# Performance work log

Measured on AMD Instinct MI355X. Metric: run time of the kernel, lower is better.

The kernel has to match this reference:

```python
import math
import jax, jax.numpy as jnp
import numpy as np

N = 100000      # nodes
E = 3200000     # edges (avg degree 32)
NFEAT = 512
NH = 256
NC = 40
NL = 8
ALPHA = 0.1
LAMDA = 0.5


def setup_inputs() -> dict:
    key = jax.random.key(0)
    ks = jax.random.split(key, 9)
    features = jax.random.normal(ks[0], (N, NFEAT), jnp.float32)
    edge_rows = jax.random.randint(ks[1], (E,), 0, N, jnp.int32)
    edge_cols = jax.random.randint(ks[2], (E,), 0, N, jnp.int32)
    # scale by 1/avg_degree so aggregated features stay O(1) (mimics normalized adjacency)
    edge_vals = jax.random.uniform(ks[3], (E,), jnp.float32) / 32.0
    # fcs[0]: nn.Linear(nfeat, nhidden) default init U(-1/sqrt(in), 1/sqrt(in))
    b1 = 1.0 / math.sqrt(NFEAT)
    W_in = jax.random.uniform(ks[4], (NFEAT, NH), jnp.float32, -b1, b1)
    b_in = jax.random.uniform(ks[5], (NH,), jnp.float32, -b1, b1)
    # GraphConvolution weights: U(-1/sqrt(out), 1/sqrt(out))
    bw = 1.0 / math.sqrt(NH)
    conv_weights = jax.random.uniform(ks[6], (NL, NH, NH), jnp.float32, -bw, bw)
    # fcs[1]: nn.Linear(nhidden, nclass)
    b2 = 1.0 / math.sqrt(NH)
    W_out = jax.random.uniform(ks[7], (NH, NC), jnp.float32, -b2, b2)
    b_out = jax.random.uniform(ks[8], (NC,), jnp.float32, -b2, b2)
    return {
        "features": features,
        "edge_rows": edge_rows,
        "edge_cols": edge_cols,
        "edge_vals": edge_vals,
        "W_in": W_in,
        "b_in": b_in,
        "conv_weights": conv_weights,
        "W_out": W_out,
        "b_out": b_out,
    }


def reference(features, edge_rows, edge_cols, edge_vals, W_in, b_in, conv_weights, W_out, b_out):
    # dropout p=0 in eval -> identity
    h = jax.nn.relu(features @ W_in + b_in)  # [N, NH]
    h0 = h
    for i in range(NL):
        theta = math.log(LAMDA / (i + 1) + 1.0)
        # SpMM: hi = G @ h via gather + segment-sum over destination rows
        hi = jax.ops.segment_sum(edge_vals[:, None] * h[edge_cols], edge_rows, num_segments=N)
        support = (1.0 - ALPHA) * hi + ALPHA * h0  # variant=False -> r == support
        h = jax.nn.relu(theta * (support @ conv_weights[i]) + (1.0 - theta) * support)
    return h @ W_out + b_out  # [N, NC]
```

## Files before the change

kernel.cpp:

```cpp
#include <hip/hip_runtime.h>
#include <hip/hip_fp16.h>
#include <math.h>

#define NNODE   100000
#define NEDGE   3200000
#define NFEAT   512
#define NH      256
#define NC      40
#define NL      8

#define SCAN_B  256

typedef _Float16 f16x8 __attribute__((ext_vector_type(8)));
typedef float    f32x4 __attribute__((ext_vector_type(4)));

__global__ void count_deg_kernel(const int* __restrict__ rows, int* __restrict__ deg, int e) {
    int i = blockIdx.x * blockDim.x + threadIdx.x;
    if (i < e) atomicAdd(&deg[rows[i]], 1);
}

__global__ void scan_pass1(const int* __restrict__ deg, int* __restrict__ rowptr,
                           int* __restrict__ bsums, int n) {
    __shared__ int sm[SCAN_B];
    int i = blockIdx.x * SCAN_B + threadIdx.x;
    int v = (i < n) ? deg[i] : 0;
    sm[threadIdx.x] = v;
    __syncthreads();
    for (int off = 1; off < SCAN_B; off <<= 1) {
        int t = (threadIdx.x >= (unsigned)off) ? sm[threadIdx.x - off] : 0;
        __syncthreads();
        sm[threadIdx.x] += t;
        __syncthreads();
    }
    if (i < n) rowptr[i] = sm[threadIdx.x] - v;
    if (threadIdx.x == SCAN_B - 1) bsums[blockIdx.x] = sm[threadIdx.x];
}

__global__ void scan_pass2(int* __restrict__ bsums, int nb) {
    __shared__ int sm[512];
    int tid = threadIdx.x;
    int v = (tid < nb) ? bsums[tid] : 0;
    sm[tid] = v;
    __syncthreads();
    for (int off = 1; off < 512; off <<= 1) {
        int t = (tid >= off) ? sm[tid - off] : 0;
        __syncthreads();
        sm[tid] += t;
        __syncthreads();
    }
    if (tid < nb) bsums[tid] = sm[tid] - v;
}

__global__ void scan_pass3(int* __restrict__ rowptr, const int* __restrict__ bsums,
                           int* __restrict__ cursor, int n, int total) {
    int i = blockIdx.x * blockDim.x + threadIdx.x;
    if (i < n) {
        int v = rowptr[i] + bsums[i / SCAN_B];
        rowptr[i] = v;
        cursor[i] = v;
    }
    if (i == 0) rowptr[n] = total;
}

__global__ void scatter_edges_kernel(const int* __restrict__ rows, const int* __restrict__ cols,
                                     const float* __restrict__ vals, int* __restrict__ cursor,
                                     int* __restrict__ csr_col, float* __restrict__ csr_val, int e) {
    int i = blockIdx.x * blockDim.x + threadIdx.x;
    if (i < e) {
        int r = rows[i];
        int p = atomicAdd(&cursor[r], 1);
        csr_col[p] = cols[i];
        csr_val[p] = vals[i];
    }
}

__device__ inline float4 dec8(uint2 p) {
    __half2 h01 = *(__half2*)&p.x;
    __half2 h23 = *(__half2*)&p.y;
    float2 f01 = __half22float2(h01);
    float2 f23 = __half22float2(h23);
    return make_float4(f01.x, f01.y, f23.x, f23.y);
}

__device__ inline void gload16(const void* g, void* l) {
    __builtin_amdgcn_global_load_lds((const __attribute__((address_space(1))) void*)g,
                                     (__attribute__((address_space(3))) void*)l,
                                     16, 0, 0);
}

__global__ void convert_f2h4(const float* __restrict__ in, __half* __restrict__ out, long n4) {
    long stride = (long)gridDim.x * blockDim.x;
    for (long i = (long)blockIdx.x * blockDim.x + threadIdx.x; i < n4; i += stride) {
        float4 f = ((const float4*)in)[i];
        __half2 a = __floats2half2_rn(f.x, f.y);
        __half2 b = __floats2half2_rn(f.z, f.w);
        uint2 pk;
        pk.x = *(unsigned*)&a;
        pk.y = *(unsigned*)&b;
        ((uint2*)out)[i] = pk;
    }
}

__global__ void convert_win(const float* __restrict__ in, __half* __restrict__ out) {
    int idx = blockIdx.x * blockDim.x + threadIdx.x;
    if (idx < NFEAT * NH) {
        int k = idx >> 8;
        int n = idx & 255;
        out[n * NFEAT + k] = __float2half(in[idx]);
    }
}

__global__ void convert_convw(const float* __restrict__ in, __half* __restrict__ out) {
    int idx = blockIdx.x * blockDim.x + threadIdx.x;
    if (idx < NL * NH * NH) {
        int l = idx >> 16;
        int rem = idx & 65535;
        int k = rem >> 8;
        int n = rem & 255;
        out[(size_t)l * 65536 + n * 256 + k] = __float2half(in[idx]);
    }
}

__global__ __launch_bounds__(256) void spmm_kernel(
    const int* __restrict__ rowptr, const int* __restrict__ csr_col,
    const float* __restrict__ csr_val, const __half* __restrict__ h16,
    const __half* __restrict__ h016,
    float* __restrict__ sup32, __half* __restrict__ sup16, int n)
{
    int lane = threadIdx.x & 63;
    int r = blockIdx.x * 4 + (threadIdx.x >> 6);
    if (r >= n) return;
    int e0 = rowptr[r], e1 = rowptr[r + 1];
    const uint2* hv = (const uint2*)h16;
    float4 acc = make_float4(0.f, 0.f, 0.f, 0.f);
    int e = e0;
    for (; e + 4 <= e1; e += 4) {
        int   c0 = csr_col[e],     c1 = csr_col[e + 1];
        int   c2 = csr_col[e + 2], c3 = csr_col[e + 3];
        float v0 = csr_val[e],     v1 = csr_val[e + 1];
        float v2 = csr_val[e + 2], v3 = csr_val[e + 3];
        uint2 p0 = hv[(size_t)c0 * 64 + lane];
        uint2 p1 = hv[(size_t)c1 * 64 + lane];
        uint2 p2 = hv[(size_t)c2 * 64 + lane];
        uint2 p3 = hv[(size_t)c3 * 64 + lane];
        float4 x0 = dec8(p0), x1 = dec8(p1), x2 = dec8(p2), x3 = dec8(p3);
        acc.x += v0 * x0.x + v1 * x1.x + v2 * x2.x + v3 * x3.x;
        acc.y += v0 * x0.y + v1 * x1.y + v2 * x2.y + v3 * x3.y;
        acc.z += v0 * x0.z + v1 * x1.z + v2 * x2.z + v3 * x3.z;
        acc.w += v0 * x0.w + v1 * x1.w + v2 * x2.w + v3 * x3.w;
    }
    for (; e < e1; ++e) {
        int c = csr_col[e];
        float v = csr_val[e];
        float4 x = dec8(hv[(size_t)c * 64 + lane]);
        acc.x += v * x.x; acc.y += v * x.y; acc.z += v * x.z; acc.w += v * x.w;
    }
    float4 s0 = dec8(((const uint2*)h016)[(size_t)r * 64 + lane]);
    float4 o;
    o.x = 0.9f * acc.x + 0.1f * s0.x;
    o.y = 0.9f * acc.y + 0.1f * s0.y;
    o.z = 0.9f * acc.z + 0.1f * s0.z;
    o.w = 0.9f * acc.w + 0.1f * s0.w;
    ((float4*)sup32)[(size_t)r * 64 + lane] = o;
    __half2 ha = __floats2half2_rn(o.x, o.y);
    __half2 hb = __floats2half2_rn(o.z, o.w);
    uint2 pk;
    pk.x = *(unsigned*)&ha;
    pk.y = *(unsigned*)&hb;
    ((uint2*)sup16)[(size_t)r * 64 + lane] = pk;
}

__global__ __launch_bounds__(256) void mfma_gemm(
    const __half* __restrict__ A, const __half* __restrict__ BT,
    const float* __restrict__ bias, const float* __restrict__ Csrc32,
    __half* __restrict__ out16, int M, int K,
    float theta, float omt, int mode)
{
    __shared__ __align__(16) char smem[32768];
    const int tid  = threadIdx.x;
    const int lane = tid & 63;
    const int w    = tid >> 6;
    const int wr   = w >> 1, wc = w & 1;
    const int bm0  = blockIdx.x * 128;
    const int bn0  = blockIdx.y * 128;
    const size_t strideAB = (size_t)K * 2;

    f32x4 acc[4][4];
    #pragma unroll
    for (int m = 0; m < 4; ++m)
        #pragma unroll
        for (int n = 0; n < 4; ++n)
            acc[m][n] = (f32x4)0.f;

    auto stage = [&](int kt, int buf) {
        const long k0b = (long)kt * 64;
        #pragma unroll
        for (int i = 0; i < 2; ++i) {
            int ia  = w * 2 + i;
            int row = ia * 16 + (lane >> 2);
            int q   = (lane & 3) * 16;
            int qs  = q ^ (((row >> 1) & 3) << 4);
            {
                int grow = bm0 + row; if (grow >= M) grow = M - 1;
                const char* g = (const char*)A + (size_t)grow * strideAB + k0b + qs;
                char* l = smem + buf * 16384 + ia * 1024;
                gload16(g, l);
            }
            {
                int gcol = bn0 + row;
                const char* g = (const char*)BT + (size_t)gcol * strideAB + k0b + qs;
                char* l = smem + buf * 16384 + 8192 + ia * 1024;
                gload16(g, l);
            }
        }
    };

    auto compute = [&](int buf) {
        const char* As = smem + buf * 16384;
        const char* Bs = As + 8192;
        const int q = (lane >> 4) * 16;
        f16x8 af[4], bf[4];
        #pragma unroll
        for (int m = 0; m < 4; ++m) {
            int row = wr * 64 + m * 16 + (lane & 15);
            af[m] = *(const f16x8*)(As + row * 64 + (q ^ (((row >> 1) & 3) << 4)));
        }
        #pragma unroll
        for (int n = 0; n < 4; ++n) {
            int col = wc * 64 + n * 16 + (lane & 15);
            bf[n] = *(const f16x8*)(Bs + col * 64 + (q ^ (((col >> 1) & 3) << 4)));
        }
        #pragma unroll
        for (int m = 0; m < 4; ++m)
            #pragma unroll
            for (int n = 0; n < 4; ++n)
                acc[m][n] = __builtin_amdgcn_mfma_f32_16x16x32_f16(af[m], bf[n], acc[m][n], 0, 0, 0);
    };

    const int nkt = K >> 5;
    stage(0, 0);
    __syncthreads();
    for (int kt = 0; kt < nkt; ++kt) {
        if (kt + 1 < nkt) stage(kt + 1, (kt + 1) & 1);
        compute(kt & 1);
        __syncthreads();
    }

    #pragma unroll
    for (int m = 0; m < 4; ++m) {
        int rbase = bm0 + wr * 64 + m * 16 + (lane >> 4) * 4;
        #pragma unroll
        for (int r = 0; r < 4; ++r) {
            int grow = rbase + r;
            if (grow >= M) continue;
            #pragma unroll
            for (int n = 0; n < 4; ++n) {
                int gcol = bn0 + wc * 64 + n * 16 + (lane & 15);
                float x = acc[m][n][r];
                if (mode == 0) {
                    x = fmaxf(x + bias[gcol], 0.f);
                } else {
                    x = fmaxf(theta * x + omt * Csrc32[(size_t)grow * 256 + gcol], 0.f);
                }
                out16[(size_t)grow * 256 + gcol] = __float2half(x);
            }
        }
    }
}

#define BM 128
#define BN 64
#define BK 16

__global__ __launch_bounds__(256) void gemm_out_kernel(
    const __half* __restrict__ A16, const float* __restrict__ B,
    const float* __restrict__ bias, float* __restrict__ out32,
    int M, int Nn, int K)
{
    __shared__ float As[BK][BM + 4];
    __shared__ float Bs[BK][BN + 4];
    int tid = threadIdx.x;
    int tx = tid & 15;
    int ty = tid >> 4;
    int bm0 = blockIdx.x * BM;
    int bn0 = blockIdx.y * BN;

    float acc[8][4];
    #pragma unroll
    for (int i = 0; i < 8; ++i)
        #pragma unroll
        for (int j = 0; j < 4; ++j) acc[i][j] = 0.f;

    for (int k0 = 0; k0 < K; k0 += BK) {
        #pragma unroll
        for (int r = 0; r < 2; ++r) {
            int idx = tid + r * 256;
            int m   = idx >> 2;
            int kk  = (idx & 3) * 4;
            int gm  = bm0 + m;
            float4 f = make_float4(0.f, 0.f, 0.f, 0.f);
            if (gm < M) f = dec8(*(const uint2*)&A16[(size_t)gm * K + k0 + kk]);
            As[kk + 0][m] = f.x;
            As[kk + 1][m] = f.y;
            As[kk + 2][m] = f.z;
            As[kk + 3][m] = f.w;
        }
        {
            int kk = tid >> 4;
            int n4 = (tid & 15) * 4;
            int gn = bn0 + n4;
            const float* brow = &B[(size_t)(k0 + kk) * Nn];
            float t0 = (gn + 0 < Nn) ? brow[gn + 0] : 0.f;
            float t1 = (gn + 1 < Nn) ? brow[gn + 1] : 0.f;
            float t2 = (gn + 2 < Nn) ? brow[gn + 2] : 0.f;
            float t3 = (gn + 3 < Nn) ? brow[gn + 3] : 0.f;
            Bs[kk][n4 + 0] = t0;
            Bs[kk][n4 + 1] = t1;
            Bs[kk][n4 + 2] = t2;
            Bs[kk][n4 + 3] = t3;
        }
        __syncthreads();
        #pragma unroll
        for (int kk = 0; kk < BK; ++kk) {
            float a[8], b[4];
            #pragma unroll
            for (int i = 0; i < 8; ++i) a[i] = As[kk][ty * 8 + i];
            #pragma unroll
            for (int j = 0; j < 4; ++j) b[j] = Bs[kk][tx * 4 + j];
            #pragma unroll
            for (int i = 0; i < 8; ++i)
                #pragma unroll
                for (int j = 0; j < 4; ++j)
                    acc[i][j] += a[i] * b[j];
        }
        __syncthreads();
    }

    #pragma unroll
    for (int i = 0; i < 8; ++i) {
        int m = bm0 + ty * 8 + i;
        if (m >= M) continue;
        int n0 = bn0 + tx * 4;
        #pragma unroll
        for (int j = 0; j < 4; ++j) {
            int n = n0 + j;
            if (n < Nn) out32[(size_t)m * Nn + n] = acc[i][j] + bias[n];
        }
    }
}

extern "C" void kernel_launch(void* const* d_in, const int* in_sizes, int n_in,
                              void* d_out, int out_size, void* d_ws, size_t ws_size,
                              hipStream_t stream) {
    const float* features = (const float*)d_in[0];
    const int*   erows    = (const int*)d_in[1];
    const int*   ecols    = (const int*)d_in[2];
    const float* evals    = (const float*)d_in[3];
    const float* W_in     = (const float*)d_in[4];
    const float* b_in     = (const float*)d_in[5];
    const float* convW    = (const float*)d_in[6];
    const float* W_out    = (const float*)d_in[7];
    const float* b_out    = (const float*)d_in[8];
    float* out = (float*)d_out;

    const int n = NNODE;
    const int e = NEDGE;

    char* w = (char*)d_ws;
    auto alloc = [&](size_t bytes) -> void* {
        void* p = (void*)w;
        w += (bytes + 255) & ~(size_t)255;
        return p;
    };
    float*  sup32   = (float*)alloc((size_t)n * NH * 4);
    __half* feat16  = (__half*)sup32;
    __half* h0_16   = (__half*)alloc((size_t)n * NH * 2);
    __half* hb_16   = (__half*)alloc((size_t)n * NH * 2);
    __half* sup16   = (__half*)alloc((size_t)n * NH * 2);
    __half* WtIn16  = (__half*)alloc((size_t)NFEAT * NH * 2);
    __half* convWt16= (__half*)alloc((size_t)NL * NH * NH * 2);
    int*    rowptr  = (int*)alloc((size_t)(n + 1) * 4);
    int*    cursor  = (int*)alloc((size_t)n * 4);
    int*    bsums   = (int*)alloc(4096 * 4);
    int*    csr_col = (int*)alloc((size_t)e * 4);
    float*  csr_val = (float*)alloc((size_t)e * 4);

    hipMemsetAsync(cursor, 0, (size_t)n * 4, stream);
    count_deg_kernel<<<(e + 255) / 256, 256, 0, stream>>>(erows, cursor, e);
    int nb = (n + SCAN_B - 1) / SCAN_B;
    scan_pass1<<<nb, SCAN_B, 0, stream>>>(cursor, rowptr, bsums, n);
    scan_pass2<<<1, 512, 0, stream>>>(bsums, nb);
    scan_pass3<<<nb, SCAN_B, 0, stream>>>(rowptr, bsums, cursor, n, e);
    scatter_edges_kernel<<<(e + 255) / 256, 256, 0, stream>>>(
        erows, ecols, evals, cursor, csr_col, csr_val, e);

    convert_f2h4<<<2048, 256, 0, stream>>>(features, feat16, (long)n * NFEAT / 4);
    convert_win<<<(NFEAT * NH + 255) / 256, 256, 0, stream>>>(W_in, WtIn16);
    convert_convw<<<(NL * NH * NH + 255) / 256, 256, 0, stream>>>(convW, convWt16);

    dim3 gmm((n + 127) / 128, 2);
    mfma_gemm<<<gmm, 256, 0, stream>>>(feat16, WtIn16, b_in, nullptr,
                                       h0_16, n, NFEAT, 0.f, 0.f, 0);

    const __half* hcur16 = h0_16;
    for (int i = 0; i < NL; ++i) {
        spmm_kernel<<<(n + 3) / 4, 256, 0, stream>>>(rowptr, csr_col, csr_val,
                                                     hcur16, h0_16, sup32, sup16, n);
        double th = log(0.5 / (double)(i + 1) + 1.0);
        mfma_gemm<<<gmm, 256, 0, stream>>>(sup16, convWt16 + (size_t)i * NH * NH,
                                           nullptr, sup32, hb_16,
                                           n, NH, (float)th, (float)(1.0 - th), 1);
        hcur16 = hb_16;
    }

    dim3 gout((n + BM - 1) / BM, (NC + BN - 1) / BN);
    gemm_out_kernel<<<gout, 256, 0, stream>>>(hb_16, W_out, b_out, out, n, NC, NH);
}
```

Before: 3.500 ms.

## Fuse feature conversion into GEMM, interleave CSR col/val, drop fp32 support buffer

The input GEMM now reads fp32 features directly and converts them to fp16 while staging into LDS. This removes the separate conversion kernel and its 100MB round trip. CSR column and value arrays are interleaved into int2 so each edge needs one load. The SpMM no longer writes an fp32 copy of support, and the GEMM epilogue reads the fp16 copy instead, which cuts about 100MB of traffic per layer at the cost of some precision in the residual term.

```diff
diff --git a/kernel.cpp b/kernel.cpp
--- a/kernel.cpp
+++ b/kernel.cpp
@@ -64,13 +64,12 @@
 
 __global__ void scatter_edges_kernel(const int* __restrict__ rows, const int* __restrict__ cols,
                                      const float* __restrict__ vals, int* __restrict__ cursor,
-                                     int* __restrict__ csr_col, float* __restrict__ csr_val, int e) {
+                                     int2* __restrict__ csr_cv, int e) {
     int i = blockIdx.x * blockDim.x + threadIdx.x;
     if (i < e) {
         int r = rows[i];
         int p = atomicAdd(&cursor[r], 1);
-        csr_col[p] = cols[i];
-        csr_val[p] = vals[i];
+        csr_cv[p] = make_int2(cols[i], __float_as_int(vals[i]));
     }
 }
 
@@ -86,19 +85,6 @@
     __builtin_amdgcn_global_load_lds((const __attribute__((address_space(1))) void*)g,
                                      (__attribute__((address_space(3))) void*)l,
                                      16, 0, 0);
-}
-
-__global__ void convert_f2h4(const float* __restrict__ in, __half* __restrict__ out, long n4) {
-    long stride = (long)gridDim.x * blockDim.x;
-    for (long i = (long)blockIdx.x * blockDim.x + threadIdx.x; i < n4; i += stride) {
-        float4 f = ((const float4*)in)[i];
-        __half2 a = __floats2half2_rn(f.x, f.y);
-        __half2 b = __floats2half2_rn(f.z, f.w);
-        uint2 pk;
-        pk.x = *(unsigned*)&a;
-        pk.y = *(unsigned*)&b;
-        ((uint2*)out)[i] = pk;
-    }
 }
 
 __global__ void convert_win(const float* __restrict__ in, __half* __restrict__ out) {
@@ -122,10 +108,9 @@
 }
 
 __global__ __launch_bounds__(256) void spmm_kernel(
-    const int* __restrict__ rowptr, const int* __restrict__ csr_col,
-    const float* __restrict__ csr_val, const __half* __restrict__ h16,
-    const __half* __restrict__ h016,
-    float* __restrict__ sup32, __half* __restrict__ sup16, int n)
+    const int* __restrict__ rowptr, const int2* __restrict__ csr_cv,
+    const __half* __restrict__ h16, const __half* __restrict__ h016,
+    __half* __restrict__ sup16, int n)
 {
     int lane = threadIdx.x & 63;
     int r = blockIdx.x * 4 + (threadIdx.x >> 6);
@@ -135,14 +120,14 @@
     float4 acc = make_float4(0.f, 0.f, 0.f, 0.f);
     int e = e0;
     for (; e + 4 <= e1; e += 4) {
-        int   c0 = csr_col[e],     c1 = csr_col[e + 1];
-        int   c2 = csr_col[e + 2], c3 = csr_col[e + 3];
-        float v0 = csr_val[e],     v1 = csr_val[e + 1];
-        float v2 = csr_val[e + 2], v3 = csr_val[e + 3];
-        uint2 p0 = hv[(size_t)c0 * 64 + lane];
-        uint2 p1 = hv[(size_t)c1 * 64 + lane];
-        uint2 p2 = hv[(size_t)c2 * 64 + lane];
-        uint2 p3 = hv[(size_t)c3 * 64 + lane];
+        int2 a0 = csr_cv[e],     a1 = csr_cv[e + 1];
+        int2 a2 = csr_cv[e + 2], a3 = csr_cv[e + 3];
+        float v0 = __int_as_float(a0.y), v1 = __int_as_float(a1.y);
+        float v2 = __int_as_float(a2.y), v3 = __int_as_float(a3.y);
+        uint2 p0 = hv[(size_t)a0.x * 64 + lane];
+        uint2 p1 = hv[(size_t)a1.x * 64 + lane];
+        uint2 p2 = hv[(size_t)a2.x * 64 + lane];
+        uint2 p3 = hv[(size_t)a3.x * 64 + lane];
         float4 x0 = dec8(p0), x1 = dec8(p1), x2 = dec8(p2), x3 = dec8(p3);
         acc.x += v0 * x0.x + v1 * x1.x + v2 * x2.x + v3 * x3.x;
         acc.y += v0 * x0.y + v1 * x1.y + v2 * x2.y + v3 * x3.y;
@@ -150,9 +135,9 @@
         acc.w += v0 * x0.w + v1 * x1.w + v2 * x2.w + v3 * x3.w;
     }
     for (; e < e1; ++e) {
-        int c = csr_col[e];
-        float v = csr_val[e];
-        float4 x = dec8(hv[(size_t)c * 64 + lane]);
+        int2 a = csr_cv[e];
+        float v = __int_as_float(a.y);
+        float4 x = dec8(hv[(size_t)a.x * 64 + lane]);
         acc.x += v * x.x; acc.y += v * x.y; acc.z += v * x.z; acc.w += v * x.w;
     }
     float4 s0 = dec8(((const uint2*)h016)[(size_t)r * 64 + lane]);
@@ -161,7 +146,6 @@
     o.y = 0.9f * acc.y + 0.1f * s0.y;
     o.z = 0.9f * acc.z + 0.1f * s0.z;
     o.w = 0.9f * acc.w + 0.1f * s0.w;
-    ((float4*)sup32)[(size_t)r * 64 + lane] = o;
     __half2 ha = __floats2half2_rn(o.x, o.y);
     __half2 hb = __floats2half2_rn(o.z, o.w);
     uint2 pk;
@@ -170,9 +154,10 @@
     ((uint2*)sup16)[(size_t)r * 64 + lane] = pk;
 }
 
+template <bool AFLOAT>
 __global__ __launch_bounds__(256) void mfma_gemm(
-    const __half* __restrict__ A, const __half* __restrict__ BT,
-    const float* __restrict__ bias, const float* __restrict__ Csrc32,
+    const void* __restrict__ Aptr, const __half* __restrict__ BT,
+    const float* __restrict__ bias, const __half* __restrict__ Csrc16,
     __half* __restrict__ out16, int M, int K,
     float theta, float omt, int mode)
 {
@@ -183,7 +168,7 @@
     const int wr   = w >> 1, wc = w & 1;
     const int bm0  = blockIdx.x * 128;
     const int bn0  = blockIdx.y * 128;
-    const size_t strideAB = (size_t)K * 2;
+    const size_t strideB = (size_t)K * 2;
 
     f32x4 acc[4][4];
     #pragma unroll
@@ -193,24 +178,49 @@
             acc[m][n] = (f32x4)0.f;
 
     auto stage = [&](int kt, int buf) {
-        const long k0b = (long)kt * 64;
-        #pragma unroll
-        for (int i = 0; i < 2; ++i) {
-            int ia  = w * 2 + i;
-            int row = ia * 16 + (lane >> 2);
-            int q   = (lane & 3) * 16;
-            int qs  = q ^ (((row >> 1) & 3) << 4);
-            {
+        if constexpr (AFLOAT) {
+            const float* A32 = (const float*)Aptr;
+            #pragma unroll
+            for (int it = 0; it < 4; ++it) {
+                int idx = tid + it * 256;
+                int r   = idx >> 3;
+                int t   = idx & 7;
+                int grow = bm0 + r; if (grow >= M) grow = M - 1;
+                float4 f = *(const float4*)&A32[(size_t)grow * K + kt * 32 + t * 4];
+                __half2 a = __floats2half2_rn(f.x, f.y);
+                __half2 b = __floats2half2_rn(f.z, f.w);
+                uint2 pk;
+                pk.x = *(unsigned*)&a;
+                pk.y = *(unsigned*)&b;
+                int slot = t >> 1;
+                int off  = r * 64 + ((slot ^ ((r >> 1) & 3)) << 4) + (t & 1) * 8;
+                *(uint2*)(smem + buf * 16384 + off) = pk;
+            }
+        } else {
+            const char* A16 = (const char*)Aptr;
+            const long k0b = (long)kt * 64;
+            #pragma unroll
+            for (int i = 0; i < 2; ++i) {
+                int ia  = w * 2 + i;
+                int row = ia * 16 + (lane >> 2);
+                int q   = (lane & 3) * 16;
+                int qs  = q ^ (((row >> 1) & 3) << 4);
                 int grow = bm0 + row; if (grow >= M) grow = M - 1;
-                const char* g = (const char*)A + (size_t)grow * strideAB + k0b + qs;
-                char* l = smem + buf * 16384 + ia * 1024;
-                gload16(g, l);
+                const char* g = A16 + (size_t)grow * strideB + k0b + qs;
+                gload16(g, smem + buf * 16384 + ia * 1024);
             }
-            {
+        }
+        {
+            const long k0b = (long)kt * 64;
+            #pragma unroll
+            for (int i = 0; i < 2; ++i) {
+                int ia  = w * 2 + i;
+                int row = ia * 16 + (lane >> 2);
+                int q   = (lane & 3) * 16;
+                int qs  = q ^ (((row >> 1) & 3) << 4);
                 int gcol = bn0 + row;
-                const char* g = (const char*)BT + (size_t)gcol * strideAB + k0b + qs;
-                char* l = smem + buf * 16384 + 8192 + ia * 1024;
-                gload16(g, l);
+                const char* g = (const char*)BT + (size_t)gcol * strideB + k0b + qs;
+                gload16(g, smem + buf * 16384 + 8192 + ia * 1024);
             }
         }
     };
@@ -260,7 +270,8 @@
                 if (mode == 0) {
                     x = fmaxf(x + bias[gcol], 0.f);
                 } else {
-                    x = fmaxf(theta * x + omt * Csrc32[(size_t)grow * 256 + gcol], 0.f);
+                    float s = __half2float(Csrc16[(size_t)grow * 256 + gcol]);
+                    x = fmaxf(theta * x + omt * s, 0.f);
                 }
                 out16[(size_t)grow * 256 + gcol] = __float2half(x);
             }
@@ -310,14 +321,10 @@
             int n4 = (tid & 15) * 4;
             int gn = bn0 + n4;
             const float* brow = &B[(size_t)(k0 + kk) * Nn];
-            float t0 = (gn + 0 < Nn) ? brow[gn + 0] : 0.f;
-            float t1 = (gn + 1 < Nn) ? brow[gn + 1] : 0.f;
-            float t2 = (gn + 2 < Nn) ? brow[gn + 2] : 0.f;
-            float t3 = (gn + 3 < Nn) ? brow[gn + 3] : 0.f;
-            Bs[kk][n4 + 0] = t0;
-            Bs[kk][n4 + 1] = t1;
-            Bs[kk][n4 + 2] = t2;
-            Bs[kk][n4 + 3] = t3;
+            Bs[kk][n4 + 0] = (gn + 0 < Nn) ? brow[gn + 0] : 0.f;
+            Bs[kk][n4 + 1] = (gn + 1 < Nn) ? brow[gn + 1] : 0.f;
+            Bs[kk][n4 + 2] = (gn + 2 < Nn) ? brow[gn + 2] : 0.f;
+            Bs[kk][n4 + 3] = (gn + 3 < Nn) ? brow[gn + 3] : 0.f;
         }
         __syncthreads();
         #pragma unroll
@@ -372,8 +379,6 @@
         w += (bytes + 255) & ~(size_t)255;
         return p;
     };
-    float*  sup32   = (float*)alloc((size_t)n * NH * 4);
-    __half* feat16  = (__half*)sup32;
     __half* h0_16   = (__half*)alloc((size_t)n * NH * 2);
     __half* hb_16   = (__half*)alloc((size_t)n * NH * 2);
     __half* sup16   = (__half*)alloc((size_t)n * NH * 2);
@@ -382,8 +387,10 @@
     int*    rowptr  = (int*)alloc((size_t)(n + 1) * 4);
     int*    cursor  = (int*)alloc((size_t)n * 4);
     int*    bsums   = (int*)alloc(4096 * 4);
-    int*    csr_col = (int*)alloc((size_t)e * 4);
-    float*  csr_val = (float*)alloc((size_t)e * 4);
+    int2*   csr_cv  = (int2*)alloc((size_t)e * 8);
+
+    convert_win<<<(NFEAT * NH + 255) / 256, 256, 0, stream>>>(W_in, WtIn16);
+    convert_convw<<<(NL * NH * NH + 255) / 256, 256, 0, stream>>>(convW, convWt16);
 
     hipMemsetAsync(cursor, 0, (size_t)n * 4, stream);
     count_deg_kernel<<<(e + 255) / 256, 256, 0, stream>>>(erows, cursor, e);
@@ -392,24 +399,20 @@
     scan_pass2<<<1, 512, 0, stream>>>(bsums, nb);
     scan_pass3<<<nb, SCAN_B, 0, stream>>>(rowptr, bsums, cursor, n, e);
     scatter_edges_kernel<<<(e + 255) / 256, 256, 0, stream>>>(
-        erows, ecols, evals, cursor, csr_col, csr_val, e);
-
-    convert_f2h4<<<2048, 256, 0, stream>>>(features, feat16, (long)n * NFEAT / 4);
-    convert_win<<<(NFEAT * NH + 255) / 256, 256, 0, stream>>>(W_in, WtIn16);
-    convert_convw<<<(NL * NH * NH + 255) / 256, 256, 0, stream>>>(convW, convWt16);
+        erows, ecols, evals, cursor, csr_cv, e);
 
     dim3 gmm((n + 127) / 128, 2);
-    mfma_gemm<<<gmm, 256, 0, stream>>>(feat16, WtIn16, b_in, nullptr,
-                                       h0_16, n, NFEAT, 0.f, 0.f, 0);
+    mfma_gemm<true><<<gmm, 256, 0, stream>>>(features, WtIn16, b_in, nullptr,
+                                             h0_16, n, NFEAT, 0.f, 0.f, 0);
 
     const __half* hcur16 = h0_16;
     for (int i = 0; i < NL; ++i) {
-        spmm_kernel<<<(n + 3) / 4, 256, 0, stream>>>(rowptr, csr_col, csr_val,
-                                                     hcur16, h0_16, sup32, sup16, n);
+        spmm_kernel<<<(n + 3) / 4, 256, 0, stream>>>(rowptr, csr_cv,
+                                                     hcur16, h0_16, sup16, n);
         double th = log(0.5 / (double)(i + 1) + 1.0);
-        mfma_gemm<<<gmm, 256, 0, stream>>>(sup16, convWt16 + (size_t)i * NH * NH,
-                                           nullptr, sup32, hb_16,
-                                           n, NH, (float)th, (float)(1.0 - th), 1);
+        mfma_gemm<false><<<gmm, 256, 0, stream>>>(sup16, convWt16 + (size_t)i * NH * NH,
+                                                  nullptr, sup16, hb_16,
+                                                  n, NH, (float)th, (float)(1.0 - th), 1);
         hcur16 = hb_16;
     }
 
```

After: 3.175 ms. 1.1x faster.
